# Optimization experiments

Hardware: AMD Instinct MI355X
Metric: run time of the kernel (lower is better)

Reference implementation:

```python
import jax, jax.numpy as jnp
import numpy as np

EPS = 1e-5

def _ln(x, s, b):
    mu = jnp.mean(x, axis=-1, keepdims=True)
    var = jnp.mean((x - mu) ** 2, axis=-1, keepdims=True)
    return (x - mu) * jax.lax.rsqrt(var + EPS) * s + b

def _gelu(x):
    return jax.nn.gelu(x, approximate=False)


def setup_inputs() -> dict:
    key = jax.random.key(0)
    ks = jax.random.split(key, 24)
    B, L, C, E, T, FC, MULT = 8, 4096, 128, 1048576, 512, 32, 2
    N = B * L
    inp = {}
    inp['feats'] = jax.random.normal(ks[0], (N, C), jnp.float32)
    inp['edge_index'] = jax.random.randint(ks[1], (2, E), 0, N, jnp.int32)
    inp['edge_attr'] = jax.random.normal(ks[2], (E, 2), jnp.float32) * 0.05  # relative coords
    inp['t'] = jax.random.normal(ks[3], (B, T), jnp.float32)
    inp['norm_vec'] = jnp.ones((N, 1), jnp.float32)
    # LayerNorms
    inp['ln1_scale'] = jnp.ones((C,), jnp.float32); inp['ln1_bias'] = jnp.zeros((C,), jnp.float32)
    inp['ln2_scale'] = jnp.ones((C,), jnp.float32); inp['ln2_bias'] = jnp.zeros((C,), jnp.float32)
    # time mlps: GELU -> Linear(T, 2C)
    sc = lambda k, sh: jax.random.normal(k, sh, jnp.float32) / np.sqrt(sh[0])
    inp['tmlp1_w'] = sc(ks[4], (T, 2 * C)); inp['tmlp1_b'] = jnp.zeros((2 * C,), jnp.float32)
    inp['tmlp2_w'] = sc(ks[5], (T, 2 * C)); inp['tmlp2_b'] = jnp.zeros((2 * C,), jnp.float32)
    # continuous-kernel MLP: 2 -> FC -> FC -> C (depthwise weights)
    inp['ker_w1'] = sc(ks[6], (2, FC)); inp['ker_b1'] = jnp.zeros((FC,), jnp.float32)
    inp['ker_w2'] = sc(ks[7], (FC, FC)); inp['ker_b2'] = jnp.zeros((FC,), jnp.float32)
    inp['ker_w3'] = sc(ks[8], (FC, C)); inp['ker_b3'] = jnp.zeros((C,), jnp.float32)
    inp['conv_bias'] = jnp.zeros((C,), jnp.float32)
    # feedforward mlp: C -> mult*C -> C
    inp['mlp_w1'] = sc(ks[9], (C, MULT * C)); inp['mlp_b1'] = jnp.zeros((MULT * C,), jnp.float32)
    inp['mlp_w2'] = sc(ks[10], (MULT * C, C)); inp['mlp_b2'] = jnp.zeros((C,), jnp.float32)
    return inp


def reference(feats, edge_index, edge_attr, t, norm_vec,
              ln1_scale, ln1_bias, ln2_scale, ln2_bias,
              tmlp1_w, tmlp1_b, tmlp2_w, tmlp2_b,
              ker_w1, ker_b1, ker_w2, ker_b2, ker_w3, ker_b3, conv_bias,
              mlp_w1, mlp_b1, mlp_w2, mlp_b2):
    N, C = feats.shape
    B = t.shape[0]
    q = N // B  # nodes per image

    def modulate(f, ln_s, ln_b, tw, tb):
        h = _ln(f, ln_s, ln_b)
        tm = _gelu(t) @ tw + tb                       # [B, 2C]
        tm = jnp.repeat(tm, q, axis=0)                # [(B q), 2C]
        scale, shift = jnp.split(tm, 2, axis=-1)
        return h * (1.0 + scale) + shift

    # pre-conv modulation
    h = modulate(feats, ln1_scale, ln1_bias, tmlp1_w, tmlp1_b)

    # continuous conv: per-edge depthwise kernel from edge_attr
    k = _gelu(edge_attr @ ker_w1 + ker_b1)
    k = _gelu(k @ ker_w2 + ker_b2)
    w = k @ ker_w3 + ker_b3                           # [E, C]
    src, dst = edge_index[0], edge_index[1]
    msg = w * h[src]                                  # gather + weight  [E, C]
    h = jax.ops.segment_sum(msg, dst, num_segments=N) + conv_bias
    h = h / norm_vec                                  # tg_div normalization

    x = feats + h                                     # residual 1

    # post-conv modulation + MLP
    h2 = modulate(x, ln2_scale, ln2_bias, tmlp2_w, tmlp2_b)
    h2 = _gelu(h2 @ mlp_w1 + mlp_b1) @ mlp_w2 + mlp_b2
    return x + h2                                     # residual 2
```

## Files before the change

### kernel.cpp

```cpp
#include <hip/hip_runtime.h>
#include <hip/hip_bf16.h>

#define C_DIM 128
#define TWO_C 256
#define FC    32
#define T_DIM 512
#define RSTR  20

typedef unsigned int   u32;
typedef unsigned short u16;
typedef unsigned long long u64;
typedef short bf16x8 __attribute__((ext_vector_type(8)));
typedef float f32x4  __attribute__((ext_vector_type(4)));

__device__ __forceinline__ float fast_rcp(float x) {
    return __builtin_amdgcn_rcpf(x);
}
__device__ __forceinline__ float gelu_f(float x) {
    float a = fabsf(x);
    float p = 1.0f + a * (0.19685352f + a * (0.11519450f +
              a * (3.4364302e-4f + a * 0.019527027f)));
    float d  = fast_rcp(p);
    float d2 = d * d;
    float d4 = d2 * d2;
    float s = 0.5f * x;
    return s + s * copysignf(1.0f - d4, x);
}
__device__ __forceinline__ u32 f2bf_bits(float x) {
    u32 u = __float_as_uint(x);
    return (u + 0x7fffu + ((u >> 16) & 1u)) >> 16;
}
__device__ __forceinline__ u32 pack_bf2(float lo, float hi) {
    __hip_bfloat162 p = __float22bfloat162_rn(make_float2(lo, hi));
    u32 r; __builtin_memcpy(&r, &p, 4); return r;
}
__device__ __forceinline__ float bf2f(u16 v) {
    return __uint_as_float((u32)v << 16);
}
__device__ __forceinline__ int hperm(int c) {
    return ((c >> 5) << 5) + ((c & 15) << 1) + ((c >> 4) & 1);
}

__global__ __launch_bounds__(256) void k_tmod(const float* __restrict__ t,
                                              const float* __restrict__ tw1,
                                              const float* __restrict__ tb1,
                                              float* __restrict__ tm1,
                                              const float* __restrict__ tw2,
                                              const float* __restrict__ tb2,
                                              float* __restrict__ tm2) {
    const float* tw = blockIdx.y ? tw2 : tw1;
    const float* tb = blockIdx.y ? tb2 : tb1;
    float*       tm = blockIdx.y ? tm2 : tm1;
    __shared__ float gt[T_DIM];
    int b = blockIdx.x;
    for (int k = threadIdx.x; k < T_DIM; k += 256)
        gt[k] = gelu_f(t[(size_t)b * T_DIM + k]);
    __syncthreads();
    int j = threadIdx.x;
    float acc = tb[j];
    for (int k = 0; k < T_DIM; ++k)
        acc += gt[k] * tw[(size_t)k * TWO_C + j];
    tm[(size_t)b * TWO_C + j] = acc;
}

template <bool BF16OUT, bool ZROW, bool PERM>
__global__ __launch_bounds__(C_DIM) void k_mod(const float* __restrict__ in,
                                               const float* __restrict__ lns,
                                               const float* __restrict__ lnb,
                                               const float* __restrict__ tm,
                                               void* __restrict__ outp, int q, int N) {
    int n = blockIdx.x, c = threadIdx.x;
    if (ZROW && n == N) {
        ((u16*)outp)[(size_t)N * C_DIM + c] = 0;
        return;
    }
    size_t o = (size_t)n * C_DIM + c;
    float v = in[o];
    float s1 = v, s2 = v * v;
#pragma unroll
    for (int off = 32; off > 0; off >>= 1) {
        s1 += __shfl_down(s1, off);
        s2 += __shfl_down(s2, off);
    }
    __shared__ float red[4];
    if ((c & 63) == 0) { red[(c >> 6) * 2] = s1; red[(c >> 6) * 2 + 1] = s2; }
    __syncthreads();
    float mean = (red[0] + red[2]) * (1.0f / C_DIM);
    float ex2  = (red[1] + red[3]) * (1.0f / C_DIM);
    float r    = rsqrtf(ex2 - mean * mean + 1e-5f);
    int b = n / q;
    float scale = tm[(size_t)b * TWO_C + c];
    float shift = tm[(size_t)b * TWO_C + C_DIM + c];
    float h = (v - mean) * r * lns[c] + lnb[c];
    float res = h * (1.0f + scale) + shift;
    if (BF16OUT) {
        int idx = PERM ? hperm(c) : c;
        ((u16*)outp)[(size_t)n * C_DIM + idx] = (u16)f2bf_bits(res);
    } else {
        ((float*)outp)[o] = res;
    }
}

__global__ void k_hist(const int* __restrict__ dst, int* __restrict__ cnt,
                       int* __restrict__ rank, int E) {
    int e = blockIdx.x * 256 + threadIdx.x;
    if (e < E) rank[e] = atomicAdd(&cnt[dst[e]], 1);
}

__global__ __launch_bounds__(1024) void k_scan_bsum(const int* __restrict__ cnt,
                                                    u64* __restrict__ bsum, int N) {
    __shared__ u64 red[1024];
    int t = threadIdx.x;
    int idx = blockIdx.x * 1024 + t;
    int v = (idx < N) ? cnt[idx] : 0;
    red[t] = (u64)(u32)v | ((u64)(u32)((v + 15) >> 4) << 32);
    __syncthreads();
#pragma unroll
    for (int off = 512; off > 0; off >>= 1) {
        if (t < off) red[t] += red[t + off];
        __syncthreads();
    }
    if (t == 0) bsum[blockIdx.x] = red[0];
}

__global__ __launch_bounds__(1024) void k_scan_btop(u64* __restrict__ bsum,
                                                    int* __restrict__ Ttot, int nb) {
    __shared__ u64 tot[1024];
    int t = threadIdx.x;
    u64 v = (t < nb) ? bsum[t] : 0ull;
    tot[t] = v;
    __syncthreads();
    for (int off = 1; off < 1024; off <<= 1) {
        u64 a = (t >= off) ? tot[t - off] : 0ull;
        __syncthreads();
        tot[t] += a;
        __syncthreads();
    }
    if (t < nb) bsum[t] = tot[t] - v;
    if (t == 1023) Ttot[0] = (int)(tot[1023] >> 32);
}

__global__ __launch_bounds__(1024) void k_scan_final(const int* __restrict__ cnt,
                                                     const u64* __restrict__ bsum,
                                                     int* __restrict__ startn,
                                                     int4* __restrict__ tinfo, int N) {
    __shared__ u64 tot[1024];
    int t = threadIdx.x;
    int idx = blockIdx.x * 1024 + t;
    int v = (idx < N) ? cnt[idx] : 0;
    u64 pk = (u64)(u32)v | ((u64)(u32)((v + 15) >> 4) << 32);
    tot[t] = pk;
    __syncthreads();
    for (int off = 1; off < 1024; off <<= 1) {
        u64 a = (t >= off) ? tot[t - off] : 0ull;
        __syncthreads();
        tot[t] += a;
        __syncthreads();
    }
    if (idx >= N) return;
    u64 ex = tot[t] - pk + bsum[blockIdx.x];
    int rd = (int)(ex & 0xffffffffull);
    int rt = (int)(ex >> 32);
    startn[idx] = rd;
    int nt = (v + 15) >> 4;
    int e = rd + v;
    for (int k = 0; k < nt; ++k)
        tinfo[rt + k] = make_int4(idx, rd + 16 * k, e, 0);
}

__global__ __launch_bounds__(256) void k_edgek2(
        const int* __restrict__ ei,
        const int* __restrict__ rank,
        const int* __restrict__ startn,
        const float* __restrict__ ea,
        const float* __restrict__ w1, const float* __restrict__ b1,
        const u16* __restrict__ w2kf, const float* __restrict__ b2,
        u32* __restrict__ rec, int E) {
    int l = threadIdx.x & 63, wv = threadIdx.x >> 6;
    int lr = l & 15, g = l >> 4;
    int wbase = blockIdx.x * 256 + wv * 64;

    bf16x8 wb0 = *(const bf16x8*)(w2kf + (size_t)l * 8);
    bf16x8 wb1 = *(const bf16x8*)(w2kf + (size_t)(64 + l) * 8);
    f32x4 bi0, bi1;
    {
        float v0 = b2[lr], v1 = b2[16 + lr];
        bi0[0] = v0; bi0[1] = v0; bi0[2] = v0; bi0[3] = v0;
        bi1[0] = v1; bi1[1] = v1; bi1[2] = v1; bi1[3] = v1;
    }
    float w1x[8], w1y[8], b1v[8];
#pragma unroll
    for (int j = 0; j < 8; ++j) {
        w1x[j] = w1[8 * g + j];
        w1y[j] = w1[FC + 8 * g + j];
        b1v[j] = b1[8 * g + j];
    }
#pragma unroll
    for (int c = 0; c < 4; ++c) {
        int cb = wbase + 16 * c;
        int eA = cb + lr;
        float2 av = make_float2(0.f, 0.f);
        int posA = 0, srcA = 0;
        if (eA < E) {
            av = ((const float2*)ea)[eA];
            srcA = ei[eA];
            posA = startn[ei[E + eA]] + rank[eA];
        }
        union { u32 w[4]; bf16x8 v; } au;
#pragma unroll
        for (int m = 0; m < 4; ++m) {
            float v0 = gelu_f(fmaf(av.x, w1x[2 * m],     fmaf(av.y, w1y[2 * m],     b1v[2 * m])));
            float v1 = gelu_f(fmaf(av.x, w1x[2 * m + 1], fmaf(av.y, w1y[2 * m + 1], b1v[2 * m + 1])));
            au.w[m] = pack_bf2(v0, v1);
        }
        f32x4 d0 = __builtin_amdgcn_mfma_f32_16x16x32_bf16(au.v, wb0, bi0, 0, 0, 0);
        f32x4 d1 = __builtin_amdgcn_mfma_f32_16x16x32_bf16(au.v, wb1, bi1, 0, 0, 0);
#pragma unroll
        for (int r = 0; r < 4; ++r) {
            int eD = cb + 4 * g + r;
            if (eD < E) {
                int pos = __shfl(posA, 4 * g + r, 64);
                u32 pk = pack_bf2(gelu_f(d0[r]), gelu_f(d1[r]));
                rec[(size_t)pos * RSTR + lr] = pk;
                if (lr == 4 * g + r) rec[(size_t)pos * RSTR + 16] = (u32)srcA;
            }
        }
    }
}

#define PREP_TOT (32768 + 32768 + 4096 + 1024)
__global__ __launch_bounds__(256) void k_prep(const float* __restrict__ mw1,
                                              const float* __restrict__ mw2,
                                              const float* __restrict__ kw3,
                                              const float* __restrict__ kw2,
                                              u16* __restrict__ w1f,
                                              u16* __restrict__ w2f,
                                              u16* __restrict__ w3f,
                                              u16* __restrict__ w2kf) {
    int t = blockIdx.x * 256 + threadIdx.x;
    if (t < 32768) {
        int j = t & 7, l = (t >> 3) & 63, f = t >> 9;
        int ks = f & 3, nt = f >> 2;
        int k = ks * 32 + ((l >> 4) << 3) + j, n = nt * 16 + (l & 15);
        w1f[t] = (u16)f2bf_bits(mw1[(size_t)k * TWO_C + n]);
    } else if (t < 65536) {
        int t2 = t - 32768;
        int j = t2 & 7, l = (t2 >> 3) & 63, f = t2 >> 9;
        int ks = f & 7, nt = f >> 3;
        int k = ks * 32 + ((l >> 4) << 3) + j, n = nt * 16 + (l & 15);
        w2f[t2] = (u16)f2bf_bits(mw2[(size_t)k * C_DIM + n]);
    } else if (t < 69632) {
        int t3 = t - 65536;
        int j = t3 & 7, l = (t3 >> 3) & 63, nt = t3 >> 9;
        int kk = ((l >> 4) << 3) + j;
        int k = (kk >> 1) + ((kk & 1) << 4);
        int n = nt * 16 + (l & 15);
        w3f[t3] = (u16)f2bf_bits(kw3[(size_t)k * C_DIM + n]);
    } else if (t < PREP_TOT) {
        int t4 = t - 69632;
        int j = t4 & 7, l = (t4 >> 3) & 63, nt = t4 >> 9;
        int kk = ((l >> 4) << 3) + j;
        int n = nt * 16 + (l & 15);
        w2kf[t4] = (u16)f2bf_bits(kw2[(size_t)kk * FC + n]);
    }
}

__global__ __launch_bounds__(256, 5) void k_conv4(
        const u16* __restrict__ h_mod,
        const int* __restrict__ Ttot,
        const int4* __restrict__ tinfo,
        const u32* __restrict__ rec,
        const u16* __restrict__ w3f, const float* __restrict__ kb3,
        float* __restrict__ xbuf, int N) {
    int l = threadIdx.x & 63, wv = threadIdx.x >> 6;
    int lr = l & 15, g = l >> 4;

    bf16x8 w3b[8];
#pragma unroll
    for (int nt = 0; nt < 8; ++nt)
        w3b[nt] = *(const bf16x8*)(w3f + ((size_t)nt * 64 + l) * 8);
    float b3c[8];
#pragma unroll
    for (int nt = 0; nt < 8; ++nt) b3c[nt] = kb3[nt * 16 + lr];
    const f32x4 zc = {0.f, 0.f, 0.f, 0.f};
    const u32* h32 = (const u32*)h_mod;

    int T = Ttot[0];
    int nw = gridDim.x * 4;
#pragma unroll 1
    for (int t = blockIdx.x * 4 + wv; t < T; t += nw) {
        int4 ti = tinfo[t];
        int n = ti.x, p0 = ti.y, e = ti.z;
        int pa = p0 + lr;
        bf16x8 a = {0, 0, 0, 0, 0, 0, 0, 0};
        if (pa < e) a = *(const bf16x8*)(rec + (size_t)pa * RSTR + g * 4);
        int srcv[4];
#pragma unroll
        for (int r = 0; r < 4; ++r) {
            int pp = p0 + 4 * g + r;
            srcv[r] = (pp < e) ? (int)rec[(size_t)pp * RSTR + 16] : N;
        }
        const u32* h0p = h32 + (size_t)srcv[0] * 64 + lr;
        const u32* h1p = h32 + (size_t)srcv[1] * 64 + lr;
        const u32* h2p = h32 + (size_t)srcv[2] * 64 + lr;
        const u32* h3p = h32 + (size_t)srcv[3] * 64 + lr;
        float acc[8];
#pragma unroll
        for (int j = 0; j < 4; ++j) {
            f32x4 w0 = __builtin_amdgcn_mfma_f32_16x16x32_bf16(a, w3b[2 * j],     zc, 0, 0, 0);
            f32x4 w1 = __builtin_amdgcn_mfma_f32_16x16x32_bf16(a, w3b[2 * j + 1], zc, 0, 0, 0);
            u32 u0 = h0p[j * 16], u1 = h1p[j * 16], u2 = h2p[j * 16], u3 = h3p[j * 16];
            float l0 = __uint_as_float(u0 << 16), h0 = __uint_as_float(u0 & 0xffff0000u);
            float l1 = __uint_as_float(u1 << 16), h1 = __uint_as_float(u1 & 0xffff0000u);
            float l2 = __uint_as_float(u2 << 16), h2 = __uint_as_float(u2 & 0xffff0000u);
            float l3 = __uint_as_float(u3 << 16), h3 = __uint_as_float(u3 & 0xffff0000u);
            acc[2 * j]     = w0[0] * l0 + w0[1] * l1 + w0[2] * l2 + w0[3] * l3
                           + b3c[2 * j] * (l0 + l1 + l2 + l3);
            acc[2 * j + 1] = w1[0] * h0 + w1[1] * h1 + w1[2] * h2 + w1[3] * h3
                           + b3c[2 * j + 1] * (h0 + h1 + h2 + h3);
        }
#pragma unroll
        for (int nt = 0; nt < 8; ++nt) {
            acc[nt] += __shfl_xor(acc[nt], 16, 64);
            acc[nt] += __shfl_xor(acc[nt], 32, 64);
        }
        float v0 = (g == 0) ? acc[0] : (g == 1) ? acc[2] : (g == 2) ? acc[4] : acc[6];
        float v1 = (g == 0) ? acc[1] : (g == 1) ? acc[3] : (g == 2) ? acc[5] : acc[7];
        float* row = xbuf + (size_t)n * C_DIM + 32 * g + lr;
        atomicAdd(row, v0);
        atomicAdd(row + 16, v1);
    }
}

__global__ __launch_bounds__(C_DIM) void k_post(const float* __restrict__ feats,
                                                const float* __restrict__ xbuf,
                                                const float* __restrict__ cbias,
                                                const float* __restrict__ normv,
                                                const float* __restrict__ tm2,
                                                const float* __restrict__ ln2s,
                                                const float* __restrict__ ln2b,
                                                float* __restrict__ out,
                                                u16* __restrict__ xmb, int q) {
    int n = blockIdx.x, c = threadIdx.x;
    size_t o = (size_t)n * C_DIM + c;
    float v = feats[o] + (xbuf[o] + cbias[c]) * fast_rcp(normv[n]);
    out[o] = v;
    float s1 = v, s2 = v * v;
#pragma unroll
    for (int off = 32; off > 0; off >>= 1) {
        s1 += __shfl_down(s1, off);
        s2 += __shfl_down(s2, off);
    }
    __shared__ float red[4];
    if ((c & 63) == 0) { red[(c >> 6) * 2] = s1; red[(c >> 6) * 2 + 1] = s2; }
    __syncthreads();
    float mean = (red[0] + red[2]) * (1.0f / C_DIM);
    float ex2  = (red[1] + red[3]) * (1.0f / C_DIM);
    float r    = rsqrtf(ex2 - mean * mean + 1e-5f);
    int b = n / q;
    float scale = tm2[(size_t)b * TWO_C + c];
    float shift = tm2[(size_t)b * TWO_C + C_DIM + c];
    float h = (v - mean) * r * ln2s[c] + ln2b[c];
    xmb[o] = (u16)f2bf_bits(h * (1.0f + scale) + shift);
}

__global__ __launch_bounds__(256) void k_ffn2(const u16* __restrict__ xm,
                                              const u16* __restrict__ w1f,
                                              const float* __restrict__ b1,
                                              const u16* __restrict__ w2f,
                                              const float* __restrict__ b2,
                                              float* __restrict__ xio, int N) {
    __shared__ u16 sm[4][4096];
    int tid = threadIdx.x, w = tid >> 6, l = tid & 63;
    int lr = l & 15, g = l >> 4;
    int n0 = blockIdx.x * 64 + w * 16;
    u16* smw = sm[w];

    bf16x8 a[4];
    const u16* xrow = xm + (size_t)(n0 + lr) * C_DIM;
#pragma unroll
    for (int ks = 0; ks < 4; ++ks)
        a[ks] = *(const bf16x8*)(xrow + ks * 32 + g * 8);
    f32x4 acc[16];
#pragma unroll
    for (int nt = 0; nt < 16; ++nt) {
        float bv = b1[nt * 16 + lr];
        acc[nt][0] = bv; acc[nt][1] = bv; acc[nt][2] = bv; acc[nt][3] = bv;
    }
#pragma unroll
    for (int nt = 0; nt < 16; ++nt)
#pragma unroll
        for (int ks = 0; ks < 4; ++ks) {
            bf16x8 bfr = *(const bf16x8*)(w1f + ((size_t)(nt * 4 + ks) * 64 + l) * 8);
            acc[nt] = __builtin_amdgcn_mfma_f32_16x16x32_bf16(a[ks], bfr, acc[nt], 0, 0, 0);
        }
#pragma unroll
    for (int nt = 0; nt < 16; ++nt)
#pragma unroll
        for (int r = 0; r < 4; ++r) {
            int row = 4 * g + r, col = nt * 16 + lr;
            int byte = row * 512 + ((col * 2) ^ ((row & 7) << 4));
            smw[byte >> 1] = (u16)f2bf_bits(gelu_f(acc[nt][r]));
        }
    f32x4 acc2[8];
#pragma unroll
    for (int nt = 0; nt < 8; ++nt) {
        float bv = b2[nt * 16 + lr];
        acc2[nt][0] = bv; acc2[nt][1] = bv; acc2[nt][2] = bv; acc2[nt][3] = bv;
    }
#pragma unroll
    for (int ks = 0; ks < 8; ++ks) {
        int byte = lr * 512 + ((ks * 64 + g * 16) ^ ((lr & 7) << 4));
        bf16x8 a2 = *(const bf16x8*)(smw + (byte >> 1));
#pragma unroll
        for (int nt = 0; nt < 8; ++nt) {
            bf16x8 bfr = *(const bf16x8*)(w2f + ((size_t)(nt * 8 + ks) * 64 + l) * 8);
            acc2[nt] = __builtin_amdgcn_mfma_f32_16x16x32_bf16(a2, bfr, acc2[nt], 0, 0, 0);
        }
    }
#pragma unroll
    for (int nt = 0; nt < 8; ++nt)
#pragma unroll
        for (int r = 0; r < 4; ++r) {
            size_t o = (size_t)(n0 + 4 * g + r) * C_DIM + nt * 16 + lr;
            xio[o] += acc2[nt][r];
        }
}

__global__ __launch_bounds__(256) void k_edge_atomic(
        const int* __restrict__ ei, const float* __restrict__ ea,
        const float* __restrict__ w1, const float* __restrict__ b1,
        const float* __restrict__ w2, const float* __restrict__ b2,
        const float* __restrict__ w3, const float* __restrict__ b3,
        const u16* __restrict__ h_mod, float* __restrict__ xacc, int E) {
    int e = blockIdx.x * 256 + threadIdx.x;
    if (e >= E) return;
    int src = ei[e], dst = ei[E + e];
    float ax = ea[(size_t)e * 2], ay = ea[(size_t)e * 2 + 1];
    float k1[FC];
#pragma unroll
    for (int i = 0; i < FC; ++i) k1[i] = gelu_f(ax * w1[i] + ay * w1[FC + i] + b1[i]);
    float k2v[FC];
#pragma unroll
    for (int j = 0; j < FC; ++j) {
        float acc = b2[j];
#pragma unroll
        for (int i = 0; i < FC; ++i) acc += k1[i] * w2[i * FC + j];
        k2v[j] = gelu_f(acc);
    }
    const u16* hrow = h_mod + (size_t)src * C_DIM;
    float* orow = xacc + (size_t)dst * C_DIM;
    for (int c = 0; c < C_DIM; ++c) {
        float wv = b3[c];
#pragma unroll
        for (int j = 0; j < FC; ++j) wv += k2v[j] * w3[j * C_DIM + c];
        atomicAdd(&orow[c], wv * bf2f(hrow[hperm(c)]));
    }
}

__global__ void k_finish(const float* __restrict__ feats, const float* __restrict__ cbias,
                         const float* __restrict__ normv, float* __restrict__ xbuf, int NC) {
    int i = blockIdx.x * 256 + threadIdx.x;
    if (i >= NC) return;
    int c = i & (C_DIM - 1);
    int n = i >> 7;
    xbuf[i] = feats[i] + (xbuf[i] + cbias[c]) / normv[n];
}

extern "C" void kernel_launch(void* const* d_in, const int* in_sizes, int n_in,
                              void* d_out, int out_size, void* d_ws, size_t ws_size,
                              hipStream_t stream) {
    const float* feats = (const float*)d_in[0];
    const int*   ei    = (const int*)d_in[1];
    const float* ea    = (const float*)d_in[2];
    const float* t     = (const float*)d_in[3];
    const float* normv = (const float*)d_in[4];
    const float* ln1s  = (const float*)d_in[5];
    const float* ln1b  = (const float*)d_in[6];
    const float* ln2s  = (const float*)d_in[7];
    const float* ln2b  = (const float*)d_in[8];
    const float* tw1   = (const float*)d_in[9];
    const float* tb1   = (const float*)d_in[10];
    const float* tw2   = (const float*)d_in[11];
    const float* tb2   = (const float*)d_in[12];
    const float* kw1   = (const float*)d_in[13];
    const float* kb1   = (const float*)d_in[14];
    const float* kw2   = (const float*)d_in[15];
    const float* kb2   = (const float*)d_in[16];
    const float* kw3   = (const float*)d_in[17];
    const float* kb3   = (const float*)d_in[18];
    const float* cbias = (const float*)d_in[19];
    const float* mw1   = (const float*)d_in[20];
    const float* mb1   = (const float*)d_in[21];
    const float* mw2   = (const float*)d_in[22];
    const float* mb2   = (const float*)d_in[23];
    float* out = (float*)d_out;

    const int N = in_sizes[0] / C_DIM;
    const int E = in_sizes[1] / 2;
    const int B = in_sizes[3] / T_DIM;
    const int q = N / B;
    const int nb = (N + 1023) / 1024;

    char* wp = (char*)d_ws;
    auto alloc = [&](size_t bytes) -> char* {
        char* p = wp; wp += (bytes + 255) & ~(size_t)255; return p;
    };
    float* tm1    = (float*)alloc((size_t)B * TWO_C * 4);
    float* tm2    = (float*)alloc((size_t)B * TWO_C * 4);
    u16*   h_mod  = (u16*)alloc(((size_t)N + 1) * C_DIM * 2);
    u16*   xmb    = (u16*)alloc((size_t)N * C_DIM * 2);
    u16*   w1f    = (u16*)alloc((size_t)C_DIM * TWO_C * 2);
    u16*   w2f    = (u16*)alloc((size_t)TWO_C * C_DIM * 2);
    u16*   w3f    = (u16*)alloc((size_t)FC * C_DIM * 2);
    u16*   w2kf   = (u16*)alloc((size_t)FC * FC * 2);
    int*   cnt    = (int*)alloc(((size_t)N + 1) * 4);
    int*   startn = (int*)alloc((size_t)N * 4);
    int*   rank   = (int*)alloc((size_t)E * 4);
    u64*   bsum   = (u64*)alloc(((size_t)nb + 1) * 8);
    int*   Ttot   = (int*)alloc(256);
    int4*  tinfo  = (int4*)alloc(((size_t)E / 16 + N + 64) * 16);
    float* xbuf   = (float*)alloc((size_t)N * C_DIM * 4);
    size_t fixed = (size_t)(wp - (char*)d_ws);
    bool can_sort = ws_size >= fixed + ((size_t)E + 16) * RSTR * 4;
    u32* rec = (u32*)alloc(((size_t)E + 16) * RSTR * 4);

    const int eb = (E + 255) / 256;

    k_tmod<<<dim3(B, 2), 256, 0, stream>>>(t, tw1, tb1, tm1, tw2, tb2, tm2);
    k_mod<true, true, true><<<N + 1, C_DIM, 0, stream>>>(feats, ln1s, ln1b, tm1,
                                                         h_mod, q, N);
    k_prep<<<(PREP_TOT + 255) / 256, 256, 0, stream>>>(mw1, mw2, kw3, kw2,
                                                       w1f, w2f, w3f, w2kf);

    if (can_sort) {
        hipMemsetAsync(cnt, 0, ((size_t)N + 1) * 4, stream);
        k_hist<<<eb, 256, 0, stream>>>(ei + E, cnt, rank, E);
        k_scan_bsum<<<nb, 1024, 0, stream>>>(cnt, bsum, N);
        k_scan_btop<<<1, 1024, 0, stream>>>(bsum, Ttot, nb);
        k_scan_final<<<nb, 1024, 0, stream>>>(cnt, bsum, startn, tinfo, N);
        k_edgek2<<<eb, 256, 0, stream>>>(ei, rank, startn, ea, kw1, kb1, w2kf, kb2,
                                         rec, E);
        hipMemsetAsync(xbuf, 0, (size_t)N * C_DIM * 4, stream);
        k_conv4<<<3072, 256, 0, stream>>>(h_mod, Ttot, tinfo, rec,
                                          w3f, kb3, xbuf, N);
        k_post<<<N, C_DIM, 0, stream>>>(feats, xbuf, cbias, normv, tm2,
                                        ln2s, ln2b, out, xmb, q);
    } else {
        hipMemsetAsync(out, 0, (size_t)N * C_DIM * 4, stream);
        k_edge_atomic<<<eb, 256, 0, stream>>>(ei, ea, kw1, kb1, kw2, kb2, kw3, kb3,
                                              h_mod, out, E);
        int nc = N * C_DIM;
        k_finish<<<(nc + 255) / 256, 256, 0, stream>>>(feats, cbias, normv, out, nc);
        k_mod<true, false, false><<<N, C_DIM, 0, stream>>>(out, ln2s, ln2b, tm2,
                                                           xmb, q, N);
    }

    k_ffn2<<<N / 64, 256, 0, stream>>>(xmb, w1f, mb1, w2f, mb2, out, N);
}
```

Before: 246.5 us.

## Scatter compact edge records first, then compute kernel features in sorted order

The old edge kernel scattered 80-byte records (16 kernel-feature words plus the source index) to sorted positions. A new k_sed kernel now scatters only an 8-byte record per edge: edge_attr packed as bf16 plus the source index. k_edgek2s then reads these in sorted order and writes the 64-byte kernel features contiguously, so the large writes become coalesced. This costs one extra kernel launch and a lossy bf16 rounding of edge_attr before the first kernel-MLP layer, and k_conv4 now reads two separate arrays instead of one interleaved record.

Measured after the change: 256.0 us. 3.9% more time.

```diff
diff --git a/kernel.cpp b/kernel.cpp
--- a/kernel.cpp
+++ b/kernel.cpp
@@ -5,7 +5,6 @@
 #define TWO_C 256
 #define FC    32
 #define T_DIM 512
-#define RSTR  20
 
 typedef unsigned int   u32;
 typedef unsigned short u16;
@@ -168,14 +167,26 @@
         tinfo[rt + k] = make_int4(idx, rd + 16 * k, e, 0);
 }
 
-__global__ __launch_bounds__(256) void k_edgek2(
-        const int* __restrict__ ei,
-        const int* __restrict__ rank,
-        const int* __restrict__ startn,
-        const float* __restrict__ ea,
+__global__ void k_sed(const int* __restrict__ ei,
+                      const int* __restrict__ rank,
+                      const int* __restrict__ startn,
+                      const float* __restrict__ ea,
+                      uint2* __restrict__ sed2, int E) {
+    int e = blockIdx.x * 256 + threadIdx.x;
+    if (e >= E) return;
+    int pos = startn[ei[E + e]] + rank[e];
+    float2 av = ((const float2*)ea)[e];
+    uint2 v;
+    v.x = pack_bf2(av.x, av.y);
+    v.y = (u32)ei[e];
+    sed2[pos] = v;
+}
+
+__global__ __launch_bounds__(256) void k_edgek2s(
+        const uint2* __restrict__ sed2,
         const float* __restrict__ w1, const float* __restrict__ b1,
         const u16* __restrict__ w2kf, const float* __restrict__ b2,
-        u32* __restrict__ rec, int E) {
+        u32* __restrict__ k2h, int E) {
     int l = threadIdx.x & 63, wv = threadIdx.x >> 6;
     int lr = l & 15, g = l >> 4;
     int wbase = blockIdx.x * 256 + wv * 64;
@@ -198,31 +209,28 @@
 #pragma unroll
     for (int c = 0; c < 4; ++c) {
         int cb = wbase + 16 * c;
-        int eA = cb + lr;
-        float2 av = make_float2(0.f, 0.f);
-        int posA = 0, srcA = 0;
-        if (eA < E) {
-            av = ((const float2*)ea)[eA];
-            srcA = ei[eA];
-            posA = startn[ei[E + eA]] + rank[eA];
+        int pA = cb + lr;
+        float ax = 0.f, ay = 0.f;
+        if (pA < E) {
+            u32 pr = sed2[pA].x;
+            ax = bf2f((u16)(pr & 0xffffu));
+            ay = bf2f((u16)(pr >> 16));
         }
         union { u32 w[4]; bf16x8 v; } au;
 #pragma unroll
         for (int m = 0; m < 4; ++m) {
-            float v0 = gelu_f(fmaf(av.x, w1x[2 * m],     fmaf(av.y, w1y[2 * m],     b1v[2 * m])));
-            float v1 = gelu_f(fmaf(av.x, w1x[2 * m + 1], fmaf(av.y, w1y[2 * m + 1], b1v[2 * m + 1])));
+            float v0 = gelu_f(fmaf(ax, w1x[2 * m],     fmaf(ay, w1y[2 * m],     b1v[2 * m])));
+            float v1 = gelu_f(fmaf(ax, w1x[2 * m + 1], fmaf(ay, w1y[2 * m + 1], b1v[2 * m + 1])));
             au.w[m] = pack_bf2(v0, v1);
         }
         f32x4 d0 = __builtin_amdgcn_mfma_f32_16x16x32_bf16(au.v, wb0, bi0, 0, 0, 0);
         f32x4 d1 = __builtin_amdgcn_mfma_f32_16x16x32_bf16(au.v, wb1, bi1, 0, 0, 0);
 #pragma unroll
         for (int r = 0; r < 4; ++r) {
-            int eD = cb + 4 * g + r;
-            if (eD < E) {
-                int pos = __shfl(posA, 4 * g + r, 64);
+            int pD = cb + 4 * g + r;
+            if (pD < E) {
                 u32 pk = pack_bf2(gelu_f(d0[r]), gelu_f(d1[r]));
-                rec[(size_t)pos * RSTR + lr] = pk;
-                if (lr == 4 * g + r) rec[(size_t)pos * RSTR + 16] = (u32)srcA;
+                k2h[(size_t)pD * 16 + lr] = pk;
             }
         }
     }
@@ -269,7 +277,8 @@
         const u16* __restrict__ h_mod,
         const int* __restrict__ Ttot,
         const int4* __restrict__ tinfo,
-        const u32* __restrict__ rec,
+        const u32* __restrict__ k2h,
+        const uint2* __restrict__ sed2,
         const u16* __restrict__ w3f, const float* __restrict__ kb3,
         float* __restrict__ xbuf, int N) {
     int l = threadIdx.x & 63, wv = threadIdx.x >> 6;
@@ -293,12 +302,12 @@
         int n = ti.x, p0 = ti.y, e = ti.z;
         int pa = p0 + lr;
         bf16x8 a = {0, 0, 0, 0, 0, 0, 0, 0};
-        if (pa < e) a = *(const bf16x8*)(rec + (size_t)pa * RSTR + g * 4);
+        if (pa < e) a = *(const bf16x8*)(k2h + (size_t)pa * 16 + g * 4);
         int srcv[4];
 #pragma unroll
         for (int r = 0; r < 4; ++r) {
             int pp = p0 + 4 * g + r;
-            srcv[r] = (pp < e) ? (int)rec[(size_t)pp * RSTR + 16] : N;
+            srcv[r] = (pp < e) ? (int)sed2[pp].y : N;
         }
         const u32* h0p = h32 + (size_t)srcv[0] * 64 + lr;
         const u32* h1p = h32 + (size_t)srcv[1] * 64 + lr;
@@ -521,9 +530,10 @@
     int*   Ttot   = (int*)alloc(256);
     int4*  tinfo  = (int4*)alloc(((size_t)E / 16 + N + 64) * 16);
     float* xbuf   = (float*)alloc((size_t)N * C_DIM * 4);
+    uint2* sed2   = (uint2*)alloc(((size_t)E + 16) * 8);
     size_t fixed = (size_t)(wp - (char*)d_ws);
-    bool can_sort = ws_size >= fixed + ((size_t)E + 16) * RSTR * 4;
-    u32* rec = (u32*)alloc(((size_t)E + 16) * RSTR * 4);
+    bool can_sort = ws_size >= fixed + ((size_t)E + 16) * 64;
+    u32* k2h = (u32*)alloc(((size_t)E + 16) * 64);
 
     const int eb = (E + 255) / 256;
 
@@ -539,10 +549,10 @@
         k_scan_bsum<<<nb, 1024, 0, stream>>>(cnt, bsum, N);
         k_scan_btop<<<1, 1024, 0, stream>>>(bsum, Ttot, nb);
         k_scan_final<<<nb, 1024, 0, stream>>>(cnt, bsum, startn, tinfo, N);
-        k_edgek2<<<eb, 256, 0, stream>>>(ei, rank, startn, ea, kw1, kb1, w2kf, kb2,
-                                         rec, E);
+        k_sed<<<eb, 256, 0, stream>>>(ei, rank, startn, ea, sed2, E);
+        k_edgek2s<<<eb, 256, 0, stream>>>(sed2, kw1, kb1, w2kf, kb2, k2h, E);
         hipMemsetAsync(xbuf, 0, (size_t)N * C_DIM * 4, stream);
-        k_conv4<<<3072, 256, 0, stream>>>(h_mod, Ttot, tinfo, rec,
+        k_conv4<<<3072, 256, 0, stream>>>(h_mod, Ttot, tinfo, k2h, sed2,
                                           w3f, kb3, xbuf, N);
         k_post<<<N, C_DIM, 0, stream>>>(feats, xbuf, cbias, normv, tm2,
                                         ln2s, ln2b, out, xmb, q);
```
